# Performance work log

Measured on AMD Instinct MI355X. Metric: run time of the kernel, lower is better.

Reference implementation:

```python
import jax, jax.numpy as jnp
import numpy as np


def _gru_layer(x, Wih, Whh, bih, bhh):
    # x: [B, T, F]; Wih: [3H, F]; Whh: [3H, H]; gate order (PyTorch): r, z, n
    B = x.shape[0]
    H = Whh.shape[1]
    xp = jnp.einsum('btf,gf->btg', x, Wih) + bih  # [B, T, 3H], input projections precomputed

    def step(h, xt):
        gh = h @ Whh.T + bhh                      # [B, 3H]
        xr, xz, xn = jnp.split(xt, 3, axis=-1)
        hr, hz, hn = jnp.split(gh, 3, axis=-1)
        r = jax.nn.sigmoid(xr + hr)
        z = jax.nn.sigmoid(xz + hz)
        n = jnp.tanh(xn + r * hn)
        h_new = (1.0 - z) * n + z * h
        return h_new, h_new

    h0 = jnp.zeros((B, H), dtype=x.dtype)
    _, ys = jax.lax.scan(step, h0, jnp.swapaxes(xp, 0, 1))  # scan over time
    return jnp.swapaxes(ys, 0, 1)                            # [B, T, H]


def setup_inputs() -> dict:
    key = jax.random.key(0)
    ks = jax.random.split(key, 16)
    B, T, F, H, O = 64, 512, 128, 512, 128
    s_in = 1.0 / np.sqrt(F)
    s_h = 1.0 / np.sqrt(H)
    inp = {
        'x': jax.random.normal(ks[0], (B, T, F), jnp.float32),
        'Wih0': jax.random.normal(ks[1], (3 * H, F), jnp.float32) * s_in,
        'Whh0': jax.random.normal(ks[2], (3 * H, H), jnp.float32) * s_h,
        'bih0': jax.random.normal(ks[3], (3 * H,), jnp.float32) * s_h,
        'bhh0': jax.random.normal(ks[4], (3 * H,), jnp.float32) * s_h,
        'Wih1': jax.random.normal(ks[5], (3 * H, H), jnp.float32) * s_h,
        'Whh1': jax.random.normal(ks[6], (3 * H, H), jnp.float32) * s_h,
        'bih1': jax.random.normal(ks[7], (3 * H,), jnp.float32) * s_h,
        'bhh1': jax.random.normal(ks[8], (3 * H,), jnp.float32) * s_h,
        'Wih2': jax.random.normal(ks[9], (3 * H, H), jnp.float32) * s_h,
        'Whh2': jax.random.normal(ks[10], (3 * H, H), jnp.float32) * s_h,
        'bih2': jax.random.normal(ks[11], (3 * H,), jnp.float32) * s_h,
        'bhh2': jax.random.normal(ks[12], (3 * H,), jnp.float32) * s_h,
        'Wout': jax.random.normal(ks[13], (O, H), jnp.float32) * s_h,
        'bout': jax.random.normal(ks[14], (O,), jnp.float32) * s_h,
    }
    return inp


def reference(x, Wih0, Whh0, bih0, bhh0, Wih1, Whh1, bih1, bhh1,
              Wih2, Whh2, bih2, bhh2, Wout, bout):
    h = _gru_layer(x, Wih0, Whh0, bih0, bhh0)
    h = _gru_layer(h, Wih1, Whh1, bih1, bhh1)
    h = _gru_layer(h, Wih2, Whh2, bih2, bhh2)
    out = jnp.einsum('bth,oh->bto', h, Wout) + bout  # linear head, output_activation=None
    return out
```

## Files before the change

kernel.cpp:

```cpp
#include <hip/hip_runtime.h>
#include <stdint.h>
#include <math.h>

#define NB 64
#define NT 512
#define NF 128
#define NH 512
#define NO 128
#define HSTR 520

typedef short  s16x8  __attribute__((ext_vector_type(8)));
typedef float  f32x4  __attribute__((ext_vector_type(4)));
typedef float  f32x16 __attribute__((ext_vector_type(16)));

#define OFF_XBF   ((size_t)0)
#define OFF_WOUT  ((size_t)(8u<<20))
#define OFF_SEQ0  ((size_t)(12u<<20))
#define OFF_SEQ1  (OFF_SEQ0 + ((size_t)32u<<20))
#define OFF_SEQ2  (OFF_SEQ1 + ((size_t)32u<<20))
#define OFF_FLAGS (OFF_SEQ2 + ((size_t)32u<<20))

#define SMEM_BYTES 88064

__device__ __forceinline__ unsigned short f2bf(float f) {
  unsigned int u = __float_as_uint(f);
  u += 0x7fffu + ((u >> 16) & 1u);
  return (unsigned short)(u >> 16);
}

__device__ __forceinline__ unsigned int ld_flag(unsigned int* p) {
  return __hip_atomic_load(p, __ATOMIC_RELAXED, __HIP_MEMORY_SCOPE_AGENT);
}

__device__ __forceinline__ void poll4(unsigned int* line, int j, unsigned int tgt) {
  unsigned int* p = line + j*4;
  for (;;) {
    unsigned int a = ld_flag(p+0), b = ld_flag(p+1);
    unsigned int c = ld_flag(p+2), d = ld_flag(p+3);
    unsigned int m = min(min(a,b), min(c,d));
    if (m >= tgt) break;
    __builtin_amdgcn_s_sleep(1);
  }
}

__device__ __forceinline__ float sigmoid_f(float x) { return 1.f / (1.f + __expf(-x)); }
__device__ __forceinline__ float tanh_f(float x)    { return 1.f - 2.f / (__expf(2.f*x) + 1.f); }

__global__ __launch_bounds__(384, 1)
void gru_persist(const unsigned short* __restrict__ xbf,
                 unsigned short* __restrict__ seq0,
                 unsigned short* __restrict__ seq1,
                 unsigned short* __restrict__ seq2,
                 unsigned int* __restrict__ flags,
                 const float* __restrict__ Wih0, const float* __restrict__ Whh0,
                 const float* __restrict__ bih0, const float* __restrict__ bhh0,
                 const float* __restrict__ Wih1, const float* __restrict__ Whh1,
                 const float* __restrict__ bih1, const float* __restrict__ bhh1,
                 const float* __restrict__ Wih2, const float* __restrict__ Whh2,
                 const float* __restrict__ bih2, const float* __restrict__ bhh2)
{
  extern __shared__ char smem[];
  unsigned short* hA = (unsigned short*)smem;
  unsigned short* xA = (unsigned short*)(smem + 16640);
  float (*xpL)[3][16][33] = (float (*)[3][16][33])(smem + 33280);
  float (*rzL)[16][33]    = (float (*)[16][33])(smem + 45952);
  unsigned short* hout    = (unsigned short*)(smem + 50176);

  const int tid  = threadIdx.x;
  const int wid  = tid >> 6;
  const int lane = tid & 63;
  const int col  = lane & 15;
  const int quad = lane >> 4;

  const int wg = blockIdx.x;
  const int l  = wg >> 6;
  const int rr = wg & 63;
  const int bq = rr >> 4;
  const int cq = rr & 15;
  const int c0 = cq * 32;
  const int b0 = bq * 16;

  unsigned short* seqw = (l==0) ? seq0 : (l==1) ? seq1 : seq2;
  const unsigned short* seqr = (l==1) ? seq0 : (l==2) ? seq1 : (const unsigned short*)0;

  const bool isrec = (wid < 3);
  const int  g     = isrec ? wid : wid - 3;

  const float* Whh = (l==0)?Whh0:(l==1)?Whh1:Whh2;
  const float* Wih = (l==0)?Wih0:(l==1)?Wih1:Wih2;
  const float* bhh = (l==0)?bhh0:(l==1)?bhh1:bhh2;
  const float* bih = (l==0)?bih0:(l==1)?bih1:bih2;

  const float* Wsrc = isrec ? Whh : Wih;
  const int K   = isrec ? NH : ((l==0) ? NF : NH);
  const int KT  = K >> 5;
  const int KTx = (l==0) ? 4 : 16;
  const int xrow = (l==0) ? NF : NH;

  s16x8 wr0[16], wr1[16];
  #pragma unroll
  for (int kt = 0; kt < 16; ++kt) {
    if (kt < KT) {
      const float* s0 = Wsrc + (size_t)(g*NH + c0 +      col) * K + kt*32 + quad*8;
      const float* s1 = Wsrc + (size_t)(g*NH + c0 + 16 + col) * K + kt*32 + quad*8;
      s16x8 w0, w1;
      #pragma unroll
      for (int j = 0; j < 8; ++j) { w0[j] = (short)f2bf(s0[j]); w1[j] = (short)f2bf(s1[j]); }
      wr0[kt] = w0; wr1[kt] = w1;
    } else { wr0[kt] = (s16x8)0; wr1[kt] = (s16x8)0; }
  }
  const float* bb = isrec ? bhh : bih;
  const float bias0 = bb[g*NH + c0 +      col];
  const float bias1 = bb[g*NH + c0 + 16 + col];

  unsigned int* line_self = flags + (size_t)(l*4 + bq)*16;
  unsigned int* line_prev = (l > 0) ? (flags + (size_t)((l-1)*4 + bq)*16) : line_self;

  auto stage_tile = [&](unsigned short* dst, const unsigned short* srcbase,
                        int rowlen, int step, int half) {
    const int sr = (half << 3) + (lane >> 3);
    const int sc = lane & 7;
    const unsigned short* src = srcbase + ((size_t)(b0 + sr)*NT + step)*rowlen;
    const int nld = rowlen >> 6;
    s16x8 tmp[8];
    #pragma unroll
    for (int i = 0; i < 8; ++i) if (i < nld) tmp[i] = *(const s16x8*)(src + (i*8 + sc)*8);
    #pragma unroll
    for (int i = 0; i < 8; ++i) if (i < nld) *(s16x8*)&dst[sr*HSTR + (i*8 + sc)*8] = tmp[i];
  };

  if (!isrec) {
    if (l > 0 && lane < 4) poll4(line_prev, lane, 1u);
    asm volatile("" ::: "memory");
    f32x4 a0 = {0.f,0.f,0.f,0.f}, a1 = {0.f,0.f,0.f,0.f};
    const unsigned short* ar = (l==0)
        ? xbf  + (size_t)(b0+col)*NT*NF + quad*8
        : seqr + (size_t)(b0+col)*NT*NH + quad*8;
    #pragma unroll
    for (int kt = 0; kt < 16; ++kt) if (kt < KTx) {
      s16x8 a = *(const s16x8*)(ar + kt*32);
      a0 = __builtin_amdgcn_mfma_f32_16x16x32_bf16(a, wr0[kt], a0, 0, 0, 0);
      a1 = __builtin_amdgcn_mfma_f32_16x16x32_bf16(a, wr1[kt], a1, 0, 0, 0);
    }
    #pragma unroll
    for (int i = 0; i < 4; ++i) {
      int row = quad*4 + i;
      xpL[0][g][row][col]      = a0[i] + bias0;
      xpL[0][g][row][col + 16] = a1[i] + bias1;
    }
  } else if (wid < 2) {
    if (l > 0 && lane < 4) poll4(line_prev, lane, 2u);
    asm volatile("" ::: "memory");
    stage_tile(xA, (l==0) ? xbf : seqr, xrow, 1, wid);
  }
  __syncthreads();

  float hp0[4] = {0.f,0.f,0.f,0.f}, hp1[4] = {0.f,0.f,0.f,0.f};

  for (int t = 0; t < NT; ++t) {
    const int slot  = t & 1;
    const int nslot = slot ^ 1;

    f32x4 a0 = {0.f,0.f,0.f,0.f}, a1 = {0.f,0.f,0.f,0.f};

    if (isrec) {
      if (t > 0) {
        #pragma unroll
        for (int kt = 0; kt < 16; ++kt) {
          s16x8 a = *(const s16x8*)&hA[col*HSTR + kt*32 + quad*8];
          a0 = __builtin_amdgcn_mfma_f32_16x16x32_bf16(a, wr0[kt], a0, 0, 0, 0);
          a1 = __builtin_amdgcn_mfma_f32_16x16x32_bf16(a, wr1[kt], a1, 0, 0, 0);
        }
      }
      if (g < 2) {
        #pragma unroll
        for (int i = 0; i < 4; ++i) {
          int row = quad*4 + i;
          float p0 = a0[i] + xpL[slot][g][row][col]      + bias0;
          float p1 = a1[i] + xpL[slot][g][row][col + 16] + bias1;
          rzL[g][row][col]      = sigmoid_f(p0);
          rzL[g][row][col + 16] = sigmoid_f(p1);
        }
      } else {
        #pragma unroll
        for (int i = 0; i < 4; ++i) { a0[i] += bias0; a1[i] += bias1; }
      }
    } else if (t + 1 < NT) {
      #pragma unroll
      for (int kt = 0; kt < 16; ++kt) if (kt < KTx) {
        s16x8 a = *(const s16x8*)&xA[col*HSTR + kt*32 + quad*8];
        a0 = __builtin_amdgcn_mfma_f32_16x16x32_bf16(a, wr0[kt], a0, 0, 0, 0);
        a1 = __builtin_amdgcn_mfma_f32_16x16x32_bf16(a, wr1[kt], a1, 0, 0, 0);
      }
      #pragma unroll
      for (int i = 0; i < 4; ++i) {
        int row = quad*4 + i;
        xpL[nslot][g][row][col]      = a0[i] + bias0;
        xpL[nslot][g][row][col + 16] = a1[i] + bias1;
      }
    }
    __syncthreads();

    if (wid == 2) {
      #pragma unroll
      for (int i = 0; i < 4; ++i) {
        int row = quad*4 + i;
        float xn0 = xpL[slot][2][row][col];
        float xn1 = xpL[slot][2][row][col + 16];
        float rt0 = rzL[0][row][col],      rt1 = rzL[0][row][col + 16];
        float zt0 = rzL[1][row][col],      zt1 = rzL[1][row][col + 16];
        float nv0 = tanh_f(xn0 + rt0 * a0[i]);
        float nv1 = tanh_f(xn1 + rt1 * a1[i]);
        float h0 = (1.f - zt0)*nv0 + zt0*hp0[i];
        float h1 = (1.f - zt1)*nv1 + zt1*hp1[i];
        hp0[i] = h0; hp1[i] = h1;
        hout[row*32 + col]      = f2bf(h0);
        hout[row*32 + col + 16] = f2bf(h1);
      }
      asm volatile("s_waitcnt lgkmcnt(0)" ::: "memory");
      {
        int srow = lane >> 2, sch = lane & 3;
        s16x8 hv = *(const s16x8*)&hout[srow*32 + sch*8];
        unsigned short* p = seqw + ((size_t)(b0+srow)*NT + t)*NH + c0 + sch*8;
        asm volatile("global_store_dwordx4 %0, %1, off sc0 sc1" :: "v"(p), "v"(hv) : "memory");
        asm volatile("s_waitcnt vmcnt(0)" ::: "memory");
      }
      if (lane == 0)
        __hip_atomic_store(line_self + cq, (unsigned)(t + 1),
                           __ATOMIC_RELAXED, __HIP_MEMORY_SCOPE_AGENT);
    } else if (wid < 2) {
      if (t + 1 < NT) {
        if (lane < 4) poll4(line_self, lane, (unsigned)(t + 1));
        asm volatile("" ::: "memory");
        stage_tile(hA, seqw, NH, t, wid);
      }
    } else if (wid == 3 || wid == 4) {
      if (t + 2 < NT) {
        if (l > 0 && lane < 4) poll4(line_prev, lane, (unsigned)(t + 3));
        asm volatile("" ::: "memory");
        stage_tile(xA, (l==0) ? xbf : seqr, xrow, t + 2, wid - 3);
      }
    }
    __syncthreads();
  }
}

__global__ __launch_bounds__(256)
void head_gemm(const unsigned short* __restrict__ seq2,
               const unsigned short* __restrict__ woutb,
               const float* __restrict__ bout,
               float* __restrict__ out)
{
  int tid = threadIdx.x;
  int wv = tid >> 6, lane = tid & 63;
  int col = lane & 31, khi = lane >> 5;
  int id = blockIdx.x*4 + wv;
  int mt = id >> 2, nt = id & 3;
  int m0 = mt*32, n0 = nt*32;
  const unsigned short* arow = seq2  + (size_t)(m0 + col)*NH + (khi << 3);
  const unsigned short* brow = woutb + (size_t)(n0 + col)*NH + (khi << 3);
  f32x16 acc;
  #pragma unroll
  for (int i = 0; i < 16; ++i) acc[i] = 0.f;
  #pragma unroll 8
  for (int kt = 0; kt < 32; ++kt) {
    s16x8 a = *(const s16x8*)(arow + kt*16);
    s16x8 b = *(const s16x8*)(brow + kt*16);
    acc = __builtin_amdgcn_mfma_f32_32x32x16_bf16(a, b, acc, 0, 0, 0);
  }
  float bo = bout[n0 + col];
  #pragma unroll
  for (int r = 0; r < 16; ++r) {
    int row = (r & 3) + ((r >> 2) << 3) + (khi << 2);
    out[(size_t)(m0 + row)*NO + n0 + col] = acc[r] + bo;
  }
}

__global__ void cast_f32_bf16(const float* __restrict__ src,
                              unsigned short* __restrict__ dst, int n) {
  int i = blockIdx.x*blockDim.x + threadIdx.x;
  int stride = gridDim.x*blockDim.x;
  for (; i < n; i += stride) dst[i] = f2bf(src[i]);
}

extern "C" void kernel_launch(void* const* d_in, const int* in_sizes, int n_in,
                              void* d_out, int out_size, void* d_ws, size_t ws_size,
                              hipStream_t stream) {
  (void)in_sizes; (void)n_in; (void)out_size; (void)ws_size;
  const float* x    = (const float*)d_in[0];
  const float* Wih0 = (const float*)d_in[1];
  const float* Whh0 = (const float*)d_in[2];
  const float* bih0 = (const float*)d_in[3];
  const float* bhh0 = (const float*)d_in[4];
  const float* Wih1 = (const float*)d_in[5];
  const float* Whh1 = (const float*)d_in[6];
  const float* bih1 = (const float*)d_in[7];
  const float* bhh1 = (const float*)d_in[8];
  const float* Wih2 = (const float*)d_in[9];
  const float* Whh2 = (const float*)d_in[10];
  const float* bih2 = (const float*)d_in[11];
  const float* bhh2 = (const float*)d_in[12];
  const float* Wout = (const float*)d_in[13];
  const float* bout = (const float*)d_in[14];

  char* ws = (char*)d_ws;
  unsigned short* xbf  = (unsigned short*)(ws + OFF_XBF);
  unsigned short* wob  = (unsigned short*)(ws + OFF_WOUT);
  unsigned short* seq0 = (unsigned short*)(ws + OFF_SEQ0);
  unsigned short* seq1 = (unsigned short*)(ws + OFF_SEQ1);
  unsigned short* seq2 = (unsigned short*)(ws + OFF_SEQ2);
  unsigned int*   flg  = (unsigned int*)(ws + OFF_FLAGS);

  (void)hipFuncSetAttribute((const void*)gru_persist,
                            hipFuncAttributeMaxDynamicSharedMemorySize, 160*1024);

  hipMemsetAsync(ws + OFF_FLAGS, 0, 4096, stream);
  cast_f32_bf16<<<512, 256, 0, stream>>>(x, xbf, NB*NT*NF);
  cast_f32_bf16<<<64, 256, 0, stream>>>(Wout, wob, NO*NH);
  gru_persist<<<192, 384, SMEM_BYTES, stream>>>(xbf, seq0, seq1, seq2, flg,
      Wih0, Whh0, bih0, bhh0, Wih1, Whh1, bih1, bhh1, Wih2, Whh2, bih2, bhh2);
  head_gemm<<<1024, 256, 0, stream>>>(seq2, wob, bout, (float*)d_out);
}
```

Baseline: 2.966 ms.

## Place recurrence groups per XCD and sync through local L2 with global fallback

The launch grows to 256 blocks and blocks are remapped so that each 16-block recurrence group tries to land on a single XCD. At startup the blocks check this by reading the hardware XCD id. When a group is co-located, it publishes h and its step flags through the XCD-local L2 (sc0 stores and loads) instead of system-coherent writes. A spare wave then republishes the previous step with sc1 writes for the next layer to consume. Polling has an iteration budget and falls back to global flags, which adds startup handshake cost and relies on the block-to-XCD assignment assumption.

```diff
diff --git a/kernel.cpp b/kernel.cpp
--- a/kernel.cpp
+++ b/kernel.cpp
@@ -12,6 +12,7 @@
 typedef short  s16x8  __attribute__((ext_vector_type(8)));
 typedef float  f32x4  __attribute__((ext_vector_type(4)));
 typedef float  f32x16 __attribute__((ext_vector_type(16)));
+typedef unsigned int u32x4 __attribute__((ext_vector_type(4)));
 
 #define OFF_XBF   ((size_t)0)
 #define OFF_WOUT  ((size_t)(8u<<20))
@@ -21,6 +22,7 @@
 #define OFF_FLAGS (OFF_SEQ2 + ((size_t)32u<<20))
 
 #define SMEM_BYTES 88064
+#define POLL_BUDGET 1024
 
 __device__ __forceinline__ unsigned short f2bf(float f) {
   unsigned int u = __float_as_uint(f);
@@ -32,7 +34,7 @@
   return __hip_atomic_load(p, __ATOMIC_RELAXED, __HIP_MEMORY_SCOPE_AGENT);
 }
 
-__device__ __forceinline__ void poll4(unsigned int* line, int j, unsigned int tgt) {
+__device__ __forceinline__ void poll4_glb(unsigned int* line, int j, unsigned int tgt) {
   unsigned int* p = line + j*4;
   for (;;) {
     unsigned int a = ld_flag(p+0), b = ld_flag(p+1);
@@ -41,6 +43,20 @@
     if (m >= tgt) break;
     __builtin_amdgcn_s_sleep(1);
   }
+}
+
+__device__ __forceinline__ bool poll4_l2(unsigned int* line, int j, unsigned int tgt) {
+  unsigned int* p = line + j*4;
+  for (int it = 0; it < POLL_BUDGET; ++it) {
+    u32x4 v;
+    asm volatile("global_load_dwordx4 %0, %1, off sc0\n\t"
+                 "s_waitcnt vmcnt(0)"
+                 : "=&v"(v) : "v"(p) : "memory");
+    unsigned int m = min(min(v[0], v[1]), min(v[2], v[3]));
+    if (m >= tgt) return true;
+    __builtin_amdgcn_s_sleep(1);
+  }
+  return false;
 }
 
 __device__ __forceinline__ float sigmoid_f(float x) { return 1.f / (1.f + __expf(-x)); }
@@ -60,6 +76,7 @@
                  const float* __restrict__ bih2, const float* __restrict__ bhh2)
 {
   extern __shared__ char smem[];
+  __shared__ unsigned int s_fast;
   unsigned short* hA = (unsigned short*)smem;
   unsigned short* xA = (unsigned short*)(smem + 16640);
   float (*xpL)[3][16][33] = (float (*)[3][16][33])(smem + 33280);
@@ -72,13 +89,40 @@
   const int col  = lane & 15;
   const int quad = lane >> 4;
 
-  const int wg = blockIdx.x;
-  const int l  = wg >> 6;
-  const int rr = wg & 63;
-  const int bq = rr >> 4;
-  const int cq = rr & 15;
+  const int bid  = blockIdx.x;
+  const int pxcd = bid & 7;
+  if (pxcd >= 6) return;
+  const int wslot = bid >> 3;
+  const int gid  = pxcd*2 + (wslot >> 4);
+  const int cq   = wslot & 15;
+  const int l    = gid >> 2;
+  const int bq   = gid & 3;
   const int c0 = cq * 32;
   const int b0 = bq * 16;
+
+  unsigned int* recline = flags + gid*16;
+  unsigned int* recbkp  = flags + 768 + gid*16;
+  unsigned int* glbline = flags + 256 + gid*16;
+  unsigned int* prevglb = (l > 0) ? (flags + 256 + (gid-4)*16) : glbline;
+  unsigned int* xcdmap  = flags + 512;
+
+  unsigned int myxcd = (__builtin_amdgcn_s_getreg(63508) & 7u) + 1u;
+  if (tid == 0) {
+    __hip_atomic_store(&xcdmap[gid*16 + cq], myxcd,
+                       __ATOMIC_RELAXED, __HIP_MEMORY_SCOPE_AGENT);
+    unsigned int ref = 0, same = 1;
+    for (int m = 0; m < 16; ++m) {
+      unsigned int v;
+      do { v = ld_flag(&xcdmap[gid*16 + m]); } while (v == 0);
+      if (m == 0) ref = v; else same &= (v == ref);
+    }
+    int fg = (gid + 2) % 12;
+    unsigned int fv;
+    do { fv = ld_flag(&xcdmap[fg*16 + 0]); } while (fv == 0);
+    s_fast = (same && (fv != ref)) ? 1u : 0u;
+  }
+  __syncthreads();
+  const bool fastp = (s_fast != 0);
 
   unsigned short* seqw = (l==0) ? seq0 : (l==1) ? seq1 : seq2;
   const unsigned short* seqr = (l==1) ? seq0 : (l==2) ? seq1 : (const unsigned short*)0;
@@ -112,9 +156,6 @@
   const float* bb = isrec ? bhh : bih;
   const float bias0 = bb[g*NH + c0 +      col];
   const float bias1 = bb[g*NH + c0 + 16 + col];
-
-  unsigned int* line_self = flags + (size_t)(l*4 + bq)*16;
-  unsigned int* line_prev = (l > 0) ? (flags + (size_t)((l-1)*4 + bq)*16) : line_self;
 
   auto stage_tile = [&](unsigned short* dst, const unsigned short* srcbase,
                         int rowlen, int step, int half) {
@@ -130,7 +171,7 @@
   };
 
   if (!isrec) {
-    if (l > 0 && lane < 4) poll4(line_prev, lane, 1u);
+    if (l > 0 && lane < 4) poll4_glb(prevglb, lane, 1u);
     asm volatile("" ::: "memory");
     f32x4 a0 = {0.f,0.f,0.f,0.f}, a1 = {0.f,0.f,0.f,0.f};
     const unsigned short* ar = (l==0)
@@ -149,17 +190,18 @@
       xpL[0][g][row][col + 16] = a1[i] + bias1;
     }
   } else if (wid < 2) {
-    if (l > 0 && lane < 4) poll4(line_prev, lane, 2u);
+    if (l > 0 && lane < 4) poll4_glb(prevglb, lane, 2u);
     asm volatile("" ::: "memory");
     stage_tile(xA, (l==0) ? xbf : seqr, xrow, 1, wid);
   }
   __syncthreads();
 
   float hp0[4] = {0.f,0.f,0.f,0.f}, hp1[4] = {0.f,0.f,0.f,0.f};
+  bool l2poll = fastp;
 
   for (int t = 0; t < NT; ++t) {
-    const int slot  = t & 1;
-    const int nslot = slot ^ 1;
+    const int slot2 = t & 1;
+    const int nslot = slot2 ^ 1;
 
     f32x4 a0 = {0.f,0.f,0.f,0.f}, a1 = {0.f,0.f,0.f,0.f};
 
@@ -176,8 +218,8 @@
         #pragma unroll
         for (int i = 0; i < 4; ++i) {
           int row = quad*4 + i;
-          float p0 = a0[i] + xpL[slot][g][row][col]      + bias0;
-          float p1 = a1[i] + xpL[slot][g][row][col + 16] + bias1;
+          float p0 = a0[i] + xpL[slot2][g][row][col]      + bias0;
+          float p1 = a1[i] + xpL[slot2][g][row][col + 16] + bias1;
           rzL[g][row][col]      = sigmoid_f(p0);
           rzL[g][row][col + 16] = sigmoid_f(p1);
         }
@@ -205,8 +247,8 @@
       #pragma unroll
       for (int i = 0; i < 4; ++i) {
         int row = quad*4 + i;
-        float xn0 = xpL[slot][2][row][col];
-        float xn1 = xpL[slot][2][row][col + 16];
+        float xn0 = xpL[slot2][2][row][col];
+        float xn1 = xpL[slot2][2][row][col + 16];
         float rt0 = rzL[0][row][col],      rt1 = rzL[0][row][col + 16];
         float zt0 = rzL[1][row][col],      zt1 = rzL[1][row][col + 16];
         float nv0 = tanh_f(xn0 + rt0 * a0[i]);
@@ -218,30 +260,75 @@
         hout[row*32 + col + 16] = f2bf(h1);
       }
       asm volatile("s_waitcnt lgkmcnt(0)" ::: "memory");
-      {
-        int srow = lane >> 2, sch = lane & 3;
-        s16x8 hv = *(const s16x8*)&hout[srow*32 + sch*8];
-        unsigned short* p = seqw + ((size_t)(b0+srow)*NT + t)*NH + c0 + sch*8;
+      int srow = lane >> 2, sch = lane & 3;
+      s16x8 hv = *(const s16x8*)&hout[srow*32 + sch*8];
+      unsigned short* p = seqw + ((size_t)(b0+srow)*NT + t)*NH + c0 + sch*8;
+      unsigned int fv = (unsigned int)(t + 1);
+      if (fastp) {
+        *(s16x8*)p = hv;
+        asm volatile("s_waitcnt vmcnt(0)" ::: "memory");
+        if (lane == 0) {
+          unsigned int* fp = recline + cq;
+          asm volatile("global_store_dword %0, %1, off sc0" :: "v"(fp), "v"(fv) : "memory");
+          __hip_atomic_store(recbkp + cq, fv,
+                             __ATOMIC_RELAXED, __HIP_MEMORY_SCOPE_AGENT);
+        }
+      } else {
         asm volatile("global_store_dwordx4 %0, %1, off sc0 sc1" :: "v"(p), "v"(hv) : "memory");
         asm volatile("s_waitcnt vmcnt(0)" ::: "memory");
-      }
-      if (lane == 0)
-        __hip_atomic_store(line_self + cq, (unsigned)(t + 1),
-                           __ATOMIC_RELAXED, __HIP_MEMORY_SCOPE_AGENT);
+        if (lane == 0) {
+          __hip_atomic_store(recbkp + cq, fv,
+                             __ATOMIC_RELAXED, __HIP_MEMORY_SCOPE_AGENT);
+          if (l < 2)
+            __hip_atomic_store(glbline + cq, fv,
+                               __ATOMIC_RELAXED, __HIP_MEMORY_SCOPE_AGENT);
+        }
+      }
     } else if (wid < 2) {
       if (t + 1 < NT) {
-        if (lane < 4) poll4(line_self, lane, (unsigned)(t + 1));
+        if (lane < 4) {
+          unsigned int tgt = (unsigned)(t + 1);
+          if (l2poll) {
+            bool ok = poll4_l2(recline, lane, tgt);
+            if (!ok) poll4_glb(recbkp, lane, tgt);
+            if (__any(!ok)) l2poll = false;
+          } else {
+            poll4_glb(recbkp, lane, tgt);
+          }
+        }
         asm volatile("" ::: "memory");
         stage_tile(hA, seqw, NH, t, wid);
       }
     } else if (wid == 3 || wid == 4) {
       if (t + 2 < NT) {
-        if (l > 0 && lane < 4) poll4(line_prev, lane, (unsigned)(t + 3));
+        if (l > 0 && lane < 4) poll4_glb(prevglb, lane, (unsigned)(t + 3));
         asm volatile("" ::: "memory");
         stage_tile(xA, (l==0) ? xbf : seqr, xrow, t + 2, wid - 3);
       }
+    } else {
+      if (fastp && l < 2 && t >= 1) {
+        int srow = lane >> 2, sch = lane & 3;
+        unsigned short* ps = seqw + ((size_t)(b0+srow)*NT + (t-1))*NH + c0 + sch*8;
+        s16x8 hv2 = *(const s16x8*)ps;
+        asm volatile("global_store_dwordx4 %0, %1, off sc0 sc1" :: "v"(ps), "v"(hv2) : "memory");
+        asm volatile("s_waitcnt vmcnt(0)" ::: "memory");
+        if (lane == 0)
+          __hip_atomic_store(glbline + cq, (unsigned)t,
+                             __ATOMIC_RELAXED, __HIP_MEMORY_SCOPE_AGENT);
+      }
     }
     __syncthreads();
+  }
+
+  if (wid == 5 && fastp && l < 2) {
+    int srow = lane >> 2, sch = lane & 3;
+    unsigned short* ps = seqw + ((size_t)(b0+srow)*NT + (NT-1))*NH + c0 + sch*8;
+    s16x8 hv2 = *(const s16x8*)ps;
+    asm volatile("global_store_dwordx4 %0, %1, off sc0 sc1" :: "v"(ps), "v"(hv2) : "memory");
+    asm volatile("s_waitcnt vmcnt(0)" ::: "memory");
+    if (lane == 0)
+      __hip_atomic_store(glbline + cq, (unsigned)NT,
+                         __ATOMIC_RELAXED, __HIP_MEMORY_SCOPE_AGENT);
   }
 }
 
@@ -317,7 +404,7 @@
   hipMemsetAsync(ws + OFF_FLAGS, 0, 4096, stream);
   cast_f32_bf16<<<512, 256, 0, stream>>>(x, xbf, NB*NT*NF);
   cast_f32_bf16<<<64, 256, 0, stream>>>(Wout, wob, NO*NH);
-  gru_persist<<<192, 384, SMEM_BYTES, stream>>>(xbf, seq0, seq1, seq2, flg,
+  gru_persist<<<256, 384, SMEM_BYTES, stream>>>(xbf, seq0, seq1, seq2, flg,
       Wih0, Whh0, bih0, bhh0, Wih1, Whh1, bih1, bhh1, Wih2, Whh2, bih2, bhh2);
   head_gemm<<<1024, 256, 0, stream>>>(seq2, wob, bout, (float*)d_out);
 }
```

Measured after the change: 4.931 ms. +66.2%, slower.
